# Performance work log

Hardware: AMD Instinct MI355X
Metric: run time of the kernel (lower is better)

Reference implementation:

```python
import jax, jax.numpy as jnp
import numpy as np
import math

B, S, D, H, F, E, K, L, V = 1, 2048, 768, 12, 1536, 8, 2, 2, 32000


def _ln(x, w, b, eps=1e-5):
    m = x.mean(-1, keepdims=True)
    v = ((x - m) ** 2).mean(-1, keepdims=True)
    return (x - m) / jnp.sqrt(v + eps) * w + b


def setup_inputs() -> dict:
    key = jax.random.key(0)
    ks = jax.random.split(key, 16)
    std = 0.02
    inp = {
        'tokens': jax.random.randint(ks[0], (B, S), 0, V),
        'emb': jax.random.normal(ks[1], (V, D), jnp.float32) * std,
        'qkv_w': jax.random.normal(ks[2], (L, 3 * D, D), jnp.float32) * std,
        'qkv_b': jax.random.normal(ks[3], (L, 3 * D), jnp.float32) * std,
        'out_w': jax.random.normal(ks[4], (L, D, D), jnp.float32) * std,
        'out_b': jax.random.normal(ks[5], (L, D), jnp.float32) * std,
        'ln1_w': jnp.ones((L, D), jnp.float32),
        'ln1_b': jax.random.normal(ks[6], (L, D), jnp.float32) * std,
        'ln2_w': jnp.ones((L, D), jnp.float32),
        'ln2_b': jax.random.normal(ks[7], (L, D), jnp.float32) * std,
        'gate_w': jax.random.normal(ks[8], (L, E, D), jnp.float32) * std,
        'eg_w': jax.random.normal(ks[9], (L, E, F, D), jnp.float32) * std,
        'eu_w': jax.random.normal(ks[10], (L, E, F, D), jnp.float32) * std,
        'ed_w': jax.random.normal(ks[11], (L, E, D, F), jnp.float32) * std,
        'rms_w': jnp.ones((D,), jnp.float32),
    }
    return inp


def reference(tokens, emb, qkv_w, qkv_b, out_w, out_b, ln1_w, ln1_b,
              ln2_w, ln2_b, gate_w, eg_w, eu_w, ed_w, rms_w):
    Dh = D // H
    x = emb[tokens] * math.sqrt(D)  # (B,S,D)
    for l in range(L):
        # --- MultiheadAttention (batch_first, no mask, eval) ---
        qkv = x @ qkv_w[l].T + qkv_b[l]
        q, k, v = jnp.split(qkv, 3, axis=-1)
        q = q.reshape(B, S, H, Dh).transpose(0, 2, 1, 3)
        k = k.reshape(B, S, H, Dh).transpose(0, 2, 1, 3)
        v = v.reshape(B, S, H, Dh).transpose(0, 2, 1, 3)
        att = jax.nn.softmax(jnp.einsum('bhqd,bhkd->bhqk', q, k) / math.sqrt(Dh), axis=-1)
        o = jnp.einsum('bhqk,bhkd->bhqd', att, v).transpose(0, 2, 1, 3).reshape(B, S, D)
        o = o @ out_w[l].T + out_b[l]
        x = _ln(x + o, ln1_w[l], ln1_b[l])
        # --- SimpleDeepseekV3MoE: top-k gate, softmax over top-k scores ---
        gs = jnp.einsum('bsd,ed->bse', x, gate_w[l])
        topv, topi = jax.lax.top_k(gs, K)
        tw = jax.nn.softmax(topv, axis=-1)  # (B,S,K)
        # dense per-expert combine weight (0 for unselected experts)
        ew = jnp.sum(jax.nn.one_hot(topi, E, dtype=x.dtype) * tw[..., None], axis=-2)  # (B,S,E)
        hg = jax.nn.silu(jnp.einsum('bsd,efd->bsef', x, eg_w[l]))
        hu = jnp.einsum('bsd,efd->bsef', x, eu_w[l])
        ye = jnp.einsum('bsef,edf->bsed', hg * hu, ed_w[l])
        moe = jnp.einsum('bsed,bse->bsd', ye, ew)
        x = _ln(x + moe, ln2_w[l], ln2_b[l])
    # final RMSNorm (torch default eps=None -> finfo eps)
    rms = jnp.sqrt(jnp.mean(x * x, axis=-1, keepdims=True) + jnp.finfo(x.dtype).eps)
    x = x / rms * rms_w
    logits = x @ emb.T  # tied lm_head
    return logits
```

## Files before the change

### kernel.cpp

```cpp
#include <hip/hip_runtime.h>

#define SQ   2048
#define DM   768
#define NHD  12
#define DHD  64
#define FF   1536
#define NE   8
#define NL   2
#define NV   32000

typedef __attribute__((ext_vector_type(8))) short bf16x8;
typedef __attribute__((ext_vector_type(4))) float f32x4;

__device__ __forceinline__ unsigned short f2bf(float f) {
  unsigned u = __float_as_uint(f);
  return (unsigned short)((u + 0x7fffu + ((u >> 16) & 1u)) >> 16);
}
__device__ __forceinline__ float bf2f(unsigned short h) {
  return __uint_as_float(((unsigned)h) << 16);
}

#define GLD16(ldsp, gp) __builtin_amdgcn_global_load_lds( \
    (const __attribute__((address_space(1))) void*)(gp),  \
    (__attribute__((address_space(3))) void*)(ldsp), 16, 0, 0)

__device__ __forceinline__ void conv8(const float* s, unsigned short* d) {
  float4 a = *(const float4*)s;
  float4 b = *(const float4*)(s + 4);
  int4 pk = make_int4(
      (int)((unsigned)f2bf(a.x) | ((unsigned)f2bf(a.y) << 16)),
      (int)((unsigned)f2bf(a.z) | ((unsigned)f2bf(a.w) << 16)),
      (int)((unsigned)f2bf(b.x) | ((unsigned)f2bf(b.y) << 16)),
      (int)((unsigned)f2bf(b.z) | ((unsigned)f2bf(b.w) << 16)));
  *(int4*)d = pk;
}

__global__ __launch_bounds__(256) void conv_embed_k(const int* __restrict__ tok,
    const float* __restrict__ emb, unsigned short* __restrict__ emb_bf,
    float* __restrict__ x, unsigned short* __restrict__ xbf,
    int* __restrict__ cnt) {
  int b = blockIdx.x;
  if (b < 12000) {
    size_t i = (size_t)(b * 256 + threadIdx.x) * 8;
    conv8(emb + i, emb_bf + i);
  } else {
    if (b == 12000 && threadIdx.x < NE) cnt[threadIdx.x] = 0;
    int idx = (b - 12000) * 256 + threadIdx.x;
    int s = idx / DM, d = idx % DM;
    float v = emb[(size_t)tok[s] * DM + d] * 27.712812921102035f;
    x[idx] = v;
    xbf[idx] = f2bf(v);
  }
}

__global__ __launch_bounds__(256) void conv5_k(const float* __restrict__ s0,
    const float* __restrict__ s1, const float* __restrict__ s2,
    const float* __restrict__ s3, const float* __restrict__ s4,
    unsigned short* __restrict__ d) {
  int b = blockIdx.x;
  const float* s; int sb;
  if (b < 864)        { s = s0; sb = b; }
  else if (b < 1152)  { s = s1; sb = b - 864; }
  else if (b < 5760)  { s = s2; sb = b - 1152; }
  else if (b < 10368) { s = s3; sb = b - 5760; }
  else                { s = s4; sb = b - 10368; }
  size_t di = (size_t)b * 2048 + threadIdx.x * 8;
  size_t si = (size_t)sb * 2048 + threadIdx.x * 8;
  conv8(s + si, d + di);
}

__global__ __launch_bounds__(512, 1) void gemmr_k(
    const unsigned short* __restrict__ A, long long lda,
    const unsigned short* __restrict__ B, long long ldb,
    float* __restrict__ C, long long ldc,
    int Kd, int mT)
{
  int nwg = gridDim.x, bid = blockIdx.x;
  int q = nwg >> 3, r = nwg & 7;
  int xcd = bid & 7, j = bid >> 3;
  int wid = (xcd < r ? xcd * (q + 1) : r * (q + 1) + (xcd - r) * q) + j;
  int mt = wid % mT, nt = wid / mT;
  int m0 = mt * 256, n0 = nt * 256;

  __shared__ __align__(16) unsigned short lds[4][2][8192];

  int t = threadIdx.x, w = t >> 6, lane = t & 63;
  int wm = w >> 2, wn = w & 3;
  int fr = lane & 15, ksg = lane >> 4;

  int srow = t >> 2;
  int schunk = ((t & 3) ^ ((srow >> 1) & 3)) * 8;
  const unsigned short* sa0 = A + (size_t)(m0 +       srow) * lda + schunk;
  const unsigned short* sa1 = A + (size_t)(m0 + 128 + srow) * lda + schunk;
  const unsigned short* sb0 = B + (size_t)(n0 +       srow) * ldb + schunk;
  const unsigned short* sb1 = B + (size_t)(n0 + 128 + srow) * ldb + schunk;
  int wofs = w * 512;

  int NS = Kd >> 5;
  f32x4 acc[8][4] = {};

#define STAGEV(s) { \
    int sl_ = (s) & 3; \
    long long ko_ = (long long)((s) >> 1) * 64 + ((s) & 1) * 32; \
    GLD16(&lds[sl_][0][wofs], sa0 + ko_); \
    GLD16(&lds[sl_][0][4096 + wofs], sa1 + ko_); \
    GLD16(&lds[sl_][1][wofs], sb0 + ko_); \
    GLD16(&lds[sl_][1][4096 + wofs], sb1 + ko_); }

  STAGEV(0);
  STAGEV(1);
  asm volatile("s_waitcnt vmcnt(4)" ::: "memory");
  __builtin_amdgcn_s_barrier();
  __builtin_amdgcn_sched_barrier(0);

  int ko = (ksg ^ ((fr >> 1) & 3)) * 8;
  for (int s = 0; s < NS; ++s) {
    int slot = s & 3;
    const unsigned short* Al = &lds[slot][0][0];
    const unsigned short* Bl = &lds[slot][1][0];
    bf16x8 af[8], bf[4];
    #pragma unroll
    for (int m = 0; m < 8; ++m)
      af[m] = *(const bf16x8*)&Al[(wm * 128 + m * 16 + fr) * 32 + ko];
    #pragma unroll
    for (int n = 0; n < 4; ++n)
      bf[n] = *(const bf16x8*)&Bl[(wn * 64 + n * 16 + fr) * 32 + ko];
    if (s + 2 < NS) STAGEV(s + 2);
    asm volatile("s_waitcnt lgkmcnt(0)" ::: "memory");
    __builtin_amdgcn_sched_barrier(0);
    __builtin_amdgcn_s_setprio(1);
    #pragma unroll
    for (int m = 0; m < 8; ++m)
      #pragma unroll
      for (int n = 0; n < 4; ++n)
        acc[m][n] = __builtin_amdgcn_mfma_f32_16x16x32_bf16(
            af[m], bf[n], acc[m][n], 0, 0, 0);
    __builtin_amdgcn_s_setprio(0);
    if (s + 1 < NS) {
      if (s + 2 < NS) asm volatile("s_waitcnt vmcnt(4)" ::: "memory");
      else            asm volatile("s_waitcnt vmcnt(0)" ::: "memory");
      __builtin_amdgcn_s_barrier();
      __builtin_amdgcn_sched_barrier(0);
    }
  }
#undef STAGEV

  int rb = ksg * 4;
  #pragma unroll
  for (int M = 0; M < 8; ++M)
    #pragma unroll
    for (int n = 0; n < 4; ++n)
      #pragma unroll
      for (int rr = 0; rr < 4; ++rr)
        C[(size_t)(m0 + wm * 128 + M * 16 + rb + rr) * ldc +
          (n0 + wn * 64 + n * 16 + fr)] = acc[M][n][rr];
}

template<bool GATHER, bool OBF16>
__global__ __launch_bounds__(512) void gemm256_k(
    const unsigned short* __restrict__ A, long long lda,
    const unsigned short* __restrict__ B, long long ldb, long long b_z,
    void* __restrict__ C, long long ldc, long long c_z,
    int M, int Kd, int mT, int nT, int Z, int zmod,
    const int* __restrict__ glist, long long gl_z,
    const int* __restrict__ cnt)
{
  int nwg = gridDim.x, bid = blockIdx.x;
  int q = nwg >> 3, r = nwg & 7;
  int xcd = bid & 7, j = bid >> 3;
  int wid = (xcd < r ? xcd * (q + 1) : r * (q + 1) + (xcd - r) * q) + j;
  int z = wid % Z; int rem = wid / Z;
  int mt = rem % mT, nt = rem / mT;
  int zz = z % zmod;
  int Mz = cnt ? cnt[zz] : M;
  int m0 = mt * 128, n0 = nt * 256;
  if (m0 >= Mz) return;
  (void)nT;

  const unsigned short* Bz = B + (size_t)z * b_z;

  __shared__ __align__(16) unsigned short lds[3 * 6 * 4096];

  int t = threadIdx.x, w = t >> 6, lane = t & 63;
  int wm = (w >> 2) * 64, wn = (w & 3) * 64;
  int fr = lane & 15, ksg = lane >> 4;
  int lrow = lane >> 3;
  int lchunk = ((lane & 7) ^ lrow) * 8;

  const unsigned short* sp[6];
  #pragma unroll
  for (int hh = 0; hh < 2; ++hh) {
    int gr = m0 + hh * 64 + w * 8 + lrow; if (gr >= Mz) gr = Mz - 1;
    int arow;
    if constexpr (GATHER) arow = glist[(size_t)zz * gl_z + gr]; else arow = gr;
    sp[hh] = A + (size_t)arow * lda + lchunk;
  }
  #pragma unroll
  for (int hh = 0; hh < 4; ++hh)
    sp[2 + hh] = Bz + (size_t)(n0 + hh * 64 + w * 8 + lrow) * ldb + lchunk;

  int rdA = (w >> 2) * 4096;
  int rdB = (2 + (w & 3)) * 4096;
  int stDst = w * 512;

  int rx = fr & 7;
  int off0 = (ksg ^ rx) * 8;
  int off1 = ((4 + ksg) ^ rx) * 8;

  int KT = Kd >> 6;
  f32x4 acc[4][4] = {};

  #pragma unroll
  for (int h = 0; h < 6; ++h)
    GLD16(&lds[h * 4096 + stDst], sp[h]);
  #pragma unroll
  for (int h = 0; h < 6; ++h)
    GLD16(&lds[(6 + h) * 4096 + stDst], sp[h] + 64);
  asm volatile("s_waitcnt vmcnt(6)" ::: "memory");
  __builtin_amdgcn_s_barrier();
  __builtin_amdgcn_sched_barrier(0);

  int buf = 0;
  for (int kt = 0; kt < KT; ++kt) {
    const unsigned short* Abl = &lds[buf * 6 * 4096 + rdA];
    const unsigned short* Bbl = &lds[buf * 6 * 4096 + rdB];
    int pf = (kt + 2 < KT);
    int pbuf = buf + 2; if (pbuf >= 3) pbuf -= 3;
    unsigned short* pd = &lds[pbuf * 6 * 4096 + stDst];
    long long koff = (long long)(kt + 2) * 64;

    if (pf) {
      GLD16(pd + 0 * 4096, sp[0] + koff);
      GLD16(pd + 1 * 4096, sp[1] + koff);
      GLD16(pd + 2 * 4096, sp[2] + koff);
    }
    {
      bf16x8 af[4], bv[4];
      #pragma unroll
      for (int m = 0; m < 4; ++m)
        af[m] = *(const bf16x8*)&Abl[(m * 16 + fr) * 64 + off0];
      #pragma unroll
      for (int n = 0; n < 4; ++n)
        bv[n] = *(const bf16x8*)&Bbl[(n * 16 + fr) * 64 + off0];
      __builtin_amdgcn_s_setprio(1);
      #pragma unroll
      for (int m = 0; m < 4; ++m)
        #pragma unroll
        for (int n = 0; n < 4; ++n)
          acc[m][n] = __builtin_amdgcn_mfma_f32_16x16x32_bf16(
              af[m], bv[n], acc[m][n], 0, 0, 0);
      __builtin_amdgcn_s_setprio(0);
    }
    if (pf) {
      GLD16(pd + 3 * 4096, sp[3] + koff);
      GLD16(pd + 4 * 4096, sp[4] + koff);
      GLD16(pd + 5 * 4096, sp[5] + koff);
    }
    {
      bf16x8 af[4], bv[4];
      #pragma unroll
      for (int m = 0; m < 4; ++m)
        af[m] = *(const bf16x8*)&Abl[(m * 16 + fr) * 64 + off1];
      #pragma unroll
      for (int n = 0; n < 4; ++n)
        bv[n] = *(const bf16x8*)&Bbl[(n * 16 + fr) * 64 + off1];
      __builtin_amdgcn_s_setprio(1);
      #pragma unroll
      for (int m = 0; m < 4; ++m)
        #pragma unroll
        for (int n = 0; n < 4; ++n)
          acc[m][n] = __builtin_amdgcn_mfma_f32_16x16x32_bf16(
              af[m], bv[n], acc[m][n], 0, 0, 0);
      __builtin_amdgcn_s_setprio(0);
    }
    if (pf) {
      asm volatile("s_waitcnt vmcnt(6)" ::: "memory");
    } else if (kt + 1 < KT) {
      asm volatile("s_waitcnt vmcnt(0)" ::: "memory");
    }
    __builtin_amdgcn_s_barrier();
    __builtin_amdgcn_sched_barrier(0);
    buf = buf + 1; if (buf == 3) buf = 0;
  }

  int rb = ksg * 4;
  #pragma unroll
  for (int m = 0; m < 4; ++m) {
    #pragma unroll
    for (int n = 0; n < 4; ++n) {
      #pragma unroll
      for (int rr = 0; rr < 4; ++rr) {
        int row = m0 + wm + m * 16 + rb + rr;
        if (row >= Mz) continue;
        size_t off = (size_t)z * c_z + (size_t)row * ldc +
                     (n0 + wn + n * 16 + fr);
        if constexpr (OBF16) ((unsigned short*)C)[off] = f2bf(acc[m][n][rr]);
        else                 ((float*)C)[off] = acc[m][n][rr];
      }
    }
  }
}

template<bool GATHER, bool BIAS, bool OBF16, bool VT>
__global__ __launch_bounds__(256) void gemm_k(
    const unsigned short* __restrict__ A, long long lda, long long a_z,
    const unsigned short* __restrict__ B, long long ldb, long long b_z,
    const float* __restrict__ bias,
    void* __restrict__ C, long long ldc, long long c_z,
    int M, int N, int Kd, float scale,
    const int* __restrict__ glist, long long gl_z,
    const int* __restrict__ cnt, int mT, int nT, int Z,
    unsigned short* __restrict__ vtout)
{
  int nwg = gridDim.x, bid = blockIdx.x;
  int q = nwg >> 3, r = nwg & 7;
  int xcd = bid & 7, j = bid >> 3;
  int wid = (xcd < r ? xcd * (q + 1) : r * (q + 1) + (xcd - r) * q) + j;
  int z = wid % Z; int rem = wid / Z;
  int mt = rem % mT, nt = rem / mT;

  int Mz = cnt ? cnt[z] : M;
  int m0 = mt * 128, n0 = nt * 128;
  if (m0 >= Mz) return;

  const unsigned short* Ab = A + (size_t)z * a_z;
  const unsigned short* Bb = B + (size_t)z * b_z;

  __shared__ __align__(16) unsigned short As[128 * 64];
  __shared__ __align__(16) unsigned short Bs[128 * 64];

  int t = threadIdx.x, w = t >> 6, lane = t & 63;
  int wm = (w >> 1) * 64, wn = (w & 1) * 64;
  int fr = lane & 15, ksg = lane >> 4;
  int lrow = lane >> 3;
  int lchunk = ((lane & 7) ^ lrow) * 8;

  const unsigned short* ap[4];
  const unsigned short* bp[4];
  unsigned short* la[4];
  unsigned short* lb[4];
  #pragma unroll
  for (int i = 0; i < 4; ++i) {
    int rrow = w * 32 + i * 8 + lrow;
    int gr = m0 + rrow; if (gr >= Mz) gr = Mz - 1;
    int arow; if constexpr (GATHER) arow = glist[(size_t)z * gl_z + gr]; else arow = gr;
    ap[i] = Ab + (size_t)arow * lda + lchunk;
    int br = n0 + rrow; if (br >= N) br = N - 1;
    bp[i] = Bb + (size_t)br * ldb + lchunk;
    la[i] = &As[(w * 32 + i * 8) * 64];
    lb[i] = &Bs[(w * 32 + i * 8) * 64];
  }

  int rx = fr & 7;
  int off0 = ((0 + ksg) ^ rx) * 8;
  int off1 = ((4 + ksg) ^ rx) * 8;

  f32x4 acc[4][4] = {};

  for (int k0 = 0; k0 < Kd; k0 += 64) {
    #pragma unroll
    for (int i = 0; i < 4; ++i) GLD16(la[i], ap[i] + k0);
    #pragma unroll
    for (int i = 0; i < 4; ++i) GLD16(lb[i], bp[i] + k0);
    __syncthreads();
    #pragma unroll
    for (int kb = 0; kb < 2; ++kb) {
      int offk = kb ? off1 : off0;
      bf16x8 af[4], bv[4];
      #pragma unroll
      for (int m = 0; m < 4; ++m)
        af[m] = *(const bf16x8*)&As[(wm + m * 16 + fr) * 64 + offk];
      #pragma unroll
      for (int n = 0; n < 4; ++n)
        bv[n] = *(const bf16x8*)&Bs[(wn + n * 16 + fr) * 64 + offk];
      #pragma unroll
      for (int m = 0; m < 4; ++m)
        #pragma unroll
        for (int n = 0; n < 4; ++n)
          acc[m][n] = __builtin_amdgcn_mfma_f32_16x16x32_bf16(
              af[m], bv[n], acc[m][n], 0, 0, 0);
    }
    __syncthreads();
  }

  int rb = ksg * 4;
  #pragma unroll
  for (int m = 0; m < 4; ++m) {
    #pragma unroll
    for (int n = 0; n < 4; ++n) {
      int col = n0 + wn + n * 16 + fr;
      if (col >= N) continue;
      #pragma unroll
      for (int rr = 0; rr < 4; ++rr) {
        int row = m0 + wm + m * 16 + rb + rr;
        if (row >= Mz) continue;
        float v = acc[m][n][rr] * scale;
        if constexpr (BIAS) v += bias[col];
        size_t off = (size_t)z * c_z + (size_t)row * ldc + col;
        if constexpr (OBF16) ((unsigned short*)C)[off] = f2bf(v);
        else                 ((float*)C)[off] = v;
        if constexpr (VT) {
          if (n0 >= 2 * DM)
            vtout[(size_t)(col - 2 * DM) * SQ + row] = f2bf(v);
        }
      }
    }
  }
}

__global__ __launch_bounds__(128) void flash_k(
    const unsigned short* __restrict__ qkv,
    const unsigned short* __restrict__ vt,
    unsigned short* __restrict__ o)
{
  int nwg = gridDim.x, bid = blockIdx.x;
  int cpx = nwg >> 3;
  int wid = (bid & 7) * cpx + (bid >> 3);
  int h  = wid >> 6;
  int qt = wid & 63;
  int q0 = qt * 32;

  __shared__ __align__(16) unsigned short Ks[128 * 64];
  __shared__ __align__(16) unsigned short Vs[128 * 64];
  __shared__ __align__(16) unsigned short Ps[2][16 * 136];

  int t = threadIdx.x, w = t >> 6, lane = t & 63;
  int fr = lane & 15, ksg = lane >> 4;
  int lrow = lane >> 3;
  int lchunk = ((lane & 7) ^ lrow) * 8;

  const unsigned short* qbase = qkv + (size_t)q0 * (3 * DM) + h * DHD;
  #pragma unroll
  for (int i = 0; i < 2; ++i) {
    int rrow = w * 16 + i * 8 + lrow;
    GLD16(&Ks[(w * 16 + i * 8) * 64], qbase + (size_t)rrow * (3 * DM) + lchunk);
  }
  __syncthreads();
  bf16x8 qf[2];
  {
    int row = w * 16 + fr, ph = fr & 7;
    qf[0] = *(const bf16x8*)&Ks[row * 64 + ((ksg ^ ph) * 8)];
    qf[1] = *(const bf16x8*)&Ks[row * 64 + (((4 + ksg) ^ ph) * 8)];
  }
  __syncthreads();

  const unsigned short* kbase = qkv + DM + h * DHD;
  const unsigned short* vb = vt + (size_t)(h * DHD) * SQ;

  f32x4 oacc[4] = {};
  float m_r[4] = {-1e30f, -1e30f, -1e30f, -1e30f};
  float l_r[4] = {0.f, 0.f, 0.f, 0.f};

  for (int kt = 0; kt < SQ / 128; ++kt) {
    int kk0 = kt * 128;
    #pragma unroll
    for (int i = 0; i < 8; ++i) {
      int rrow = w * 64 + i * 8 + lrow;
      GLD16(&Ks[(w * 64 + i * 8) * 64],
            kbase + (size_t)(kk0 + rrow) * (3 * DM) + lchunk);
    }
    #pragma unroll
    for (int i = 0; i < 8; ++i) {
      int p = w * 64 + i * 8 + lrow;
      GLD16(&Vs[(w * 64 + i * 8) * 64],
            vb + (size_t)(p >> 1) * SQ + kk0 + (p & 1) * 64 + lchunk);
    }
    __syncthreads();

    f32x4 sacc[8] = {};
    __builtin_amdgcn_s_setprio(1);
    #pragma unroll
    for (int kb = 0; kb < 2; ++kb) {
      #pragma unroll
      for (int n = 0; n < 8; ++n) {
        int row = n * 16 + fr;
        bf16x8 bvv = *(const bf16x8*)&Ks[row * 64 +
            (((kb * 4 + ksg) ^ (fr & 7)) * 8)];
        sacc[n] = __builtin_amdgcn_mfma_f32_16x16x32_bf16(
            qf[kb], bvv, sacc[n], 0, 0, 0);
      }
    }
    __builtin_amdgcn_s_setprio(0);

    #pragma unroll
    for (int r = 0; r < 4; ++r) {
      float mx = sacc[0][r];
      #pragma unroll
      for (int n = 1; n < 8; ++n) mx = fmaxf(mx, sacc[n][r]);
      mx = fmaxf(mx, __shfl_xor(mx, 1));
      mx = fmaxf(mx, __shfl_xor(mx, 2));
      mx = fmaxf(mx, __shfl_xor(mx, 4));
      mx = fmaxf(mx, __shfl_xor(mx, 8));
      float mn = fmaxf(m_r[r], mx * 0.125f);
      float resc = __expf(m_r[r] - mn);
      m_r[r] = mn;
      #pragma unroll
      for (int n = 0; n < 4; ++n) oacc[n][r] *= resc;
      float rs = 0.f;
      #pragma unroll
      for (int n = 0; n < 8; ++n) {
        float p = __expf(sacc[n][r] * 0.125f - mn);
        rs += p;
        Ps[w][(ksg * 4 + r) * 136 + n * 16 + fr] = f2bf(p);
      }
      rs += __shfl_xor(rs, 1);
      rs += __shfl_xor(rs, 2);
      rs += __shfl_xor(rs, 4);
      rs += __shfl_xor(rs, 8);
      l_r[r] = l_r[r] * resc + rs;
    }

    __builtin_amdgcn_s_setprio(1);
    #pragma unroll
    for (int ksi = 0; ksi < 4; ++ksi) {
      bf16x8 pa = *(const bf16x8*)&Ps[w][fr * 136 + ksi * 32 + ksg * 8];
      #pragma unroll
      for (int n = 0; n < 4; ++n) {
        int p = (n * 16 + fr) * 2 + (ksi >> 1);
        int c = (ksi & 1) * 4 + ksg;
        bf16x8 bvv = *(const bf16x8*)&Vs[p * 64 + ((c ^ (p & 7)) * 8)];
        oacc[n] = __builtin_amdgcn_mfma_f32_16x16x32_bf16(
            pa, bvv, oacc[n], 0, 0, 0);
      }
    }
    __builtin_amdgcn_s_setprio(0);
    __syncthreads();
  }

  unsigned short* ob = o + (size_t)(q0 + w * 16) * DM + h * DHD;
  #pragma unroll
  for (int r = 0; r < 4; ++r) {
    float invl = 1.f / l_r[r];
    int qrow = ksg * 4 + r;
    #pragma unroll
    for (int n = 0; n < 4; ++n)
      ob[(size_t)qrow * DM + n * 16 + fr] = f2bf(oacc[n][r] * invl);
  }
}

__global__ __launch_bounds__(256) void add_ln_gate_k(const float* __restrict__ xin,
    const float* __restrict__ add, const float* __restrict__ w,
    const float* __restrict__ b, const float* __restrict__ gw,
    float* __restrict__ xout, unsigned short* __restrict__ xbf,
    float* __restrict__ tw, int* __restrict__ ti, int* __restrict__ cnt,
    int* __restrict__ lists, int* __restrict__ slot) {
  int row = blockIdx.x, t = threadIdx.x;
  const float* xi = xin + (size_t)row * DM;
  const float* ai = add + (size_t)row * DM;
  float v[3]; float s = 0.f, sq = 0.f;
  #pragma unroll
  for (int i = 0; i < 3; ++i) {
    int idx = t + i * 256;
    v[i] = xi[idx] + ai[idx];
    s += v[i]; sq += v[i] * v[i];
  }
  #pragma unroll
  for (int o = 32; o; o >>= 1) { s += __shfl_xor(s, o); sq += __shfl_xor(sq, o); }
  __shared__ float rsm[4], rqm[4];
  __shared__ float gsm[4][NE];
  int wv = t >> 6, lane = t & 63;
  if (lane == 0) { rsm[wv] = s; rqm[wv] = sq; }
  __syncthreads();
  s = rsm[0] + rsm[1] + rsm[2] + rsm[3];
  sq = rqm[0] + rqm[1] + rqm[2] + rqm[3];
  float mean = s * (1.f / 768.f);
  float var = sq * (1.f / 768.f) - mean * mean;
  float inv = rsqrtf(var + 1e-5f);
  float* xo = xout + (size_t)row * DM;
  unsigned short* xb = xbf + (size_t)row * DM;
  float y[3];
  #pragma unroll
  for (int i = 0; i < 3; ++i) {
    int idx = t + i * 256;
    y[i] = (v[i] - mean) * inv * w[idx] + b[idx];
    xo[idx] = y[i]; xb[idx] = f2bf(y[i]);
  }
  float p[NE];
  #pragma unroll
  for (int e = 0; e < NE; ++e) {
    p[e] = y[0] * gw[e * DM + t] + y[1] * gw[e * DM + t + 256]
         + y[2] * gw[e * DM + t + 512];
    #pragma unroll
    for (int o = 32; o; o >>= 1) p[e] += __shfl_xor(p[e], o);
  }
  if (lane == 0) {
    #pragma unroll
    for (int e = 0; e < NE; ++e) gsm[wv][e] = p[e];
  }
  __syncthreads();
  if (t == 0) {
    float v0 = -1e30f, v1 = -1e30f; int i0 = 0, i1 = 0;
    #pragma unroll
    for (int e = 0; e < NE; ++e) {
      float g = gsm[0][e] + gsm[1][e] + gsm[2][e] + gsm[3][e];
      if (g > v0) { v1 = v0; i1 = i0; v0 = g; i0 = e; }
      else if (g > v1) { v1 = g; i1 = e; }
    }
    float e1 = expf(v1 - v0);
    float invs = 1.f / (1.f + e1);
    tw[row * 2] = invs; tw[row * 2 + 1] = e1 * invs;
    ti[row * 2] = i0;   ti[row * 2 + 1] = i1;
    int p0 = atomicAdd(&cnt[i0], 1); lists[i0 * SQ + p0] = row; slot[row * 2] = p0;
    int p1 = atomicAdd(&cnt[i1], 1); lists[i1 * SQ + p1] = row; slot[row * 2 + 1] = p1;
  }
}

__global__ __launch_bounds__(256) void silu_mul_k(unsigned short* __restrict__ hg,
    const unsigned short* __restrict__ hu, const int* __restrict__ cnt) {
  int e = blockIdx.y, sl = blockIdx.x;
  if (sl >= cnt[e]) return;
  size_t base = ((size_t)e * SQ + sl) * FF;
  int t = threadIdx.x;
  #pragma unroll
  for (int i = 0; i < FF / 256; ++i) {
    size_t idx = base + t + i * 256;
    float g = bf2f(hg[idx]);
    float u = bf2f(hu[idx]);
    float sv = g / (1.f + expf(-g));
    hg[idx] = f2bf(sv * u);
  }
}

template<bool FINAL>
__global__ __launch_bounds__(256) void combine_ln_k(const float* __restrict__ xin,
    const float* __restrict__ ye, const float* __restrict__ tw,
    const int* __restrict__ ti, const int* __restrict__ slot,
    const float* __restrict__ w, const float* __restrict__ b,
    const float* __restrict__ rw,
    float* __restrict__ xout, unsigned short* __restrict__ xbf,
    int* __restrict__ cnt) {
  int row = blockIdx.x, t = threadIdx.x;
  if (!FINAL && row < NE && t == 0) cnt[row] = 0;
  int e0 = ti[row * 2], e1 = ti[row * 2 + 1];
  int p0 = slot[row * 2], p1 = slot[row * 2 + 1];
  float w0 = tw[row * 2], w1 = tw[row * 2 + 1];
  const float* y0 = ye + ((size_t)e0 * SQ + p0) * DM;
  const float* y1 = ye + ((size_t)e1 * SQ + p1) * DM;
  const float* xi = xin + (size_t)row * DM;
  float v[3]; float s = 0.f, sq = 0.f;
  #pragma unroll
  for (int i = 0; i < 3; ++i) {
    int idx = t + i * 256;
    v[i] = xi[idx] + w0 * y0[idx] + w1 * y1[idx];
    s += v[i]; sq += v[i] * v[i];
  }
  #pragma unroll
  for (int o = 32; o; o >>= 1) { s += __shfl_xor(s, o); sq += __shfl_xor(sq, o); }
  __shared__ float rsm[4], rqm[4];
  int wv = t >> 6;
  if ((t & 63) == 0) { rsm[wv] = s; rqm[wv] = sq; }
  __syncthreads();
  s = rsm[0] + rsm[1] + rsm[2] + rsm[3];
  sq = rqm[0] + rqm[1] + rqm[2] + rqm[3];
  float mean = s * (1.f / 768.f);
  float var = sq * (1.f / 768.f) - mean * mean;
  float inv = rsqrtf(var + 1e-5f);
  unsigned short* xb = xbf + (size_t)row * DM;
  float y[3];
  #pragma unroll
  for (int i = 0; i < 3; ++i) {
    int idx = t + i * 256;
    y[i] = (v[i] - mean) * inv * w[idx] + b[idx];
  }
  if constexpr (!FINAL) {
    float* xo = xout + (size_t)row * DM;
    #pragma unroll
    for (int i = 0; i < 3; ++i) {
      int idx = t + i * 256;
      xo[idx] = y[i]; xb[idx] = f2bf(y[i]);
    }
  } else {
    float sq2 = y[0] * y[0] + y[1] * y[1] + y[2] * y[2];
    #pragma unroll
    for (int o = 32; o; o >>= 1) sq2 += __shfl_xor(sq2, o);
    __syncthreads();
    if ((t & 63) == 0) rqm[wv] = sq2;
    __syncthreads();
    sq2 = rqm[0] + rqm[1] + rqm[2] + rqm[3];
    float inv2 = rsqrtf(sq2 * (1.f / 768.f) + 1.1920929e-07f);
    #pragma unroll
    for (int i = 0; i < 3; ++i) {
      int idx = t + i * 256;
      xb[idx] = f2bf(y[i] * inv2 * rw[idx]);
    }
  }
}

extern "C" void kernel_launch(void* const* d_in, const int* in_sizes, int n_in,
                              void* d_out, int out_size, void* d_ws, size_t ws_size,
                              hipStream_t stream) {
  (void)in_sizes; (void)n_in; (void)out_size; (void)ws_size;
  const int*   tokens = (const int*)d_in[0];
  const float* emb    = (const float*)d_in[1];
  const float* qkv_w  = (const float*)d_in[2];
  const float* qkv_b  = (const float*)d_in[3];
  const float* out_w  = (const float*)d_in[4];
  const float* out_b  = (const float*)d_in[5];
  const float* ln1_w  = (const float*)d_in[6];
  const float* ln1_b  = (const float*)d_in[7];
  const float* ln2_w  = (const float*)d_in[8];
  const float* ln2_b  = (const float*)d_in[9];
  const float* gate_w = (const float*)d_in[10];
  const float* eg_w   = (const float*)d_in[11];
  const float* eu_w   = (const float*)d_in[12];
  const float* ed_w   = (const float*)d_in[13];
  const float* rms_w  = (const float*)d_in[14];
  float* out = (float*)d_out;

  char* wsb = (char*)d_ws;
  float*          x_f    = (float*)(wsb + 0);
  unsigned short* x_bf   = (unsigned short*)(wsb + 6291456);
  unsigned short* qkv_bf = (unsigned short*)(wsb + 9437184);
  unsigned short* vt     = (unsigned short*)(wsb + 18874368);
  unsigned short* o_bf   = (unsigned short*)(wsb + 22020096);
  float*          tmp_f  = (float*)(wsb + 25165824);
  float*          tw     = (float*)(wsb + 31457280);
  int*            ti     = (int*)(wsb + 31473664);
  int*            cnt    = (int*)(wsb + 31490048);
  int*            lists  = (int*)(wsb + 31490304);
  int*            slot   = (int*)(wsb + 31555840);
  unsigned short* emb_bf = (unsigned short*)(wsb + 31572224);
  unsigned short* wbf    = (unsigned short*)(wsb + 80724224);
  unsigned short* hg     = (unsigned short*)(wsb + 142065920);
  unsigned short* hu     = (unsigned short*)(wsb + 142065920 + 50331648);
  float*          ye     = (float*)(wsb + 142065920 + 50331648);

  unsigned short* qw_bf = wbf;
  unsigned short* ow_bf = wbf + 1769472;
  unsigned short* eg_bf = wbf + 2359296;
  unsigned short* ed_bf = wbf + 21233664;

  conv_embed_k<<<18144, 256, 0, stream>>>(tokens, emb, emb_bf, x_f, x_bf, cnt);

  for (int l = 0; l < NL; ++l) {
    const float* qw = qkv_w + (size_t)l * 3 * DM * DM;
    const float* qb = qkv_b + (size_t)l * 3 * DM;
    const float* ow = out_w + (size_t)l * DM * DM;
    const float* ob = out_b + (size_t)l * DM;
    const float* gw = gate_w + (size_t)l * NE * DM;
    const float* egw = eg_w + (size_t)l * NE * FF * DM;
    const float* euw = eu_w + (size_t)l * NE * FF * DM;
    const float* edw = ed_w + (size_t)l * NE * DM * FF;

    conv5_k<<<14976, 256, 0, stream>>>(qw, ow, egw, euw, edw, qw_bf);

    gemm_k<false, true, true, true><<<16 * 18, 256, 0, stream>>>(
        x_bf, DM, 0, qw_bf, DM, 0, qb, qkv_bf, 3 * DM, 0,
        SQ, 3 * DM, DM, 1.f, nullptr, 0, nullptr, 16, 18, 1, vt);

    flash_k<<<NHD * 64, 128, 0, stream>>>(qkv_bf, vt, o_bf);

    gemm_k<false, true, false, false><<<16 * 6, 256, 0, stream>>>(
        o_bf, DM, 0, ow_bf, DM, 0, ob, tmp_f, DM, 0,
        SQ, DM, DM, 1.f, nullptr, 0, nullptr, 16, 6, 1, nullptr);

    add_ln_gate_k<<<SQ, 256, 0, stream>>>(x_f, tmp_f, ln1_w + l * DM,
        ln1_b + l * DM, gw, x_f, x_bf, tw, ti, cnt, lists, slot);

    gemm256_k<true, true><<<16 * 6 * 16, 512, 0, stream>>>(
        x_bf, DM, eg_bf, DM, (long long)FF * DM,
        hg, FF, (long long)SQ * FF,
        SQ, DM, 16, 6, 16, 8, lists, SQ, cnt);

    silu_mul_k<<<dim3(SQ, NE), 256, 0, stream>>>(hg, hu, cnt);

    gemm_k<false, false, false, false><<<16 * 6 * NE, 256, 0, stream>>>(
        hg, FF, (long long)SQ * FF, ed_bf, FF, (long long)DM * FF, nullptr,
        ye, DM, (long long)SQ * DM,
        SQ, DM, FF, 1.f, nullptr, 0, cnt, 16, 6, NE, nullptr);

    if (l == NL - 1)
      combine_ln_k<true><<<SQ, 256, 0, stream>>>(x_f, ye, tw, ti, slot,
          ln2_w + l * DM, ln2_b + l * DM, rms_w, x_f, x_bf, cnt);
    else
      combine_ln_k<false><<<SQ, 256, 0, stream>>>(x_f, ye, tw, ti, slot,
          ln2_w + l * DM, ln2_b + l * DM, rms_w, x_f, x_bf, cnt);
  }

  gemmr_k<<<8 * 125, 512, 0, stream>>>(
      x_bf, DM, emb_bf, DM, out, NV, DM, 8);
}
```

Measured before the change: 761.6 us.

## Fuse gate and up expert GEMMs with SiLU-multiply epilogue into one kernel

```diff
diff --git a/kernel.cpp b/kernel.cpp
--- a/kernel.cpp
+++ b/kernel.cpp
@@ -154,151 +154,6 @@
       for (int rr = 0; rr < 4; ++rr)
         C[(size_t)(m0 + wm * 128 + M * 16 + rb + rr) * ldc +
           (n0 + wn * 64 + n * 16 + fr)] = acc[M][n][rr];
-}
-
-template<bool GATHER, bool OBF16>
-__global__ __launch_bounds__(512) void gemm256_k(
-    const unsigned short* __restrict__ A, long long lda,
-    const unsigned short* __restrict__ B, long long ldb, long long b_z,
-    void* __restrict__ C, long long ldc, long long c_z,
-    int M, int Kd, int mT, int nT, int Z, int zmod,
-    const int* __restrict__ glist, long long gl_z,
-    const int* __restrict__ cnt)
-{
-  int nwg = gridDim.x, bid = blockIdx.x;
-  int q = nwg >> 3, r = nwg & 7;
-  int xcd = bid & 7, j = bid >> 3;
-  int wid = (xcd < r ? xcd * (q + 1) : r * (q + 1) + (xcd - r) * q) + j;
-  int z = wid % Z; int rem = wid / Z;
-  int mt = rem % mT, nt = rem / mT;
-  int zz = z % zmod;
-  int Mz = cnt ? cnt[zz] : M;
-  int m0 = mt * 128, n0 = nt * 256;
-  if (m0 >= Mz) return;
-  (void)nT;
-
-  const unsigned short* Bz = B + (size_t)z * b_z;
-
-  __shared__ __align__(16) unsigned short lds[3 * 6 * 4096];
-
-  int t = threadIdx.x, w = t >> 6, lane = t & 63;
-  int wm = (w >> 2) * 64, wn = (w & 3) * 64;
-  int fr = lane & 15, ksg = lane >> 4;
-  int lrow = lane >> 3;
-  int lchunk = ((lane & 7) ^ lrow) * 8;
-
-  const unsigned short* sp[6];
-  #pragma unroll
-  for (int hh = 0; hh < 2; ++hh) {
-    int gr = m0 + hh * 64 + w * 8 + lrow; if (gr >= Mz) gr = Mz - 1;
-    int arow;
-    if constexpr (GATHER) arow = glist[(size_t)zz * gl_z + gr]; else arow = gr;
-    sp[hh] = A + (size_t)arow * lda + lchunk;
-  }
-  #pragma unroll
-  for (int hh = 0; hh < 4; ++hh)
-    sp[2 + hh] = Bz + (size_t)(n0 + hh * 64 + w * 8 + lrow) * ldb + lchunk;
-
-  int rdA = (w >> 2) * 4096;
-  int rdB = (2 + (w & 3)) * 4096;
-  int stDst = w * 512;
-
-  int rx = fr & 7;
-  int off0 = (ksg ^ rx) * 8;
-  int off1 = ((4 + ksg) ^ rx) * 8;
-
-  int KT = Kd >> 6;
-  f32x4 acc[4][4] = {};
-
-  #pragma unroll
-  for (int h = 0; h < 6; ++h)
-    GLD16(&lds[h * 4096 + stDst], sp[h]);
-  #pragma unroll
-  for (int h = 0; h < 6; ++h)
-    GLD16(&lds[(6 + h) * 4096 + stDst], sp[h] + 64);
-  asm volatile("s_waitcnt vmcnt(6)" ::: "memory");
-  __builtin_amdgcn_s_barrier();
-  __builtin_amdgcn_sched_barrier(0);
-
-  int buf = 0;
-  for (int kt = 0; kt < KT; ++kt) {
-    const unsigned short* Abl = &lds[buf * 6 * 4096 + rdA];
-    const unsigned short* Bbl = &lds[buf * 6 * 4096 + rdB];
-    int pf = (kt + 2 < KT);
-    int pbuf = buf + 2; if (pbuf >= 3) pbuf -= 3;
-    unsigned short* pd = &lds[pbuf * 6 * 4096 + stDst];
-    long long koff = (long long)(kt + 2) * 64;
-
-    if (pf) {
-      GLD16(pd + 0 * 4096, sp[0] + koff);
-      GLD16(pd + 1 * 4096, sp[1] + koff);
-      GLD16(pd + 2 * 4096, sp[2] + koff);
-    }
-    {
-      bf16x8 af[4], bv[4];
-      #pragma unroll
-      for (int m = 0; m < 4; ++m)
-        af[m] = *(const bf16x8*)&Abl[(m * 16 + fr) * 64 + off0];
-      #pragma unroll
-      for (int n = 0; n < 4; ++n)
-        bv[n] = *(const bf16x8*)&Bbl[(n * 16 + fr) * 64 + off0];
-      __builtin_amdgcn_s_setprio(1);
-      #pragma unroll
-      for (int m = 0; m < 4; ++m)
-        #pragma unroll
-        for (int n = 0; n < 4; ++n)
-          acc[m][n] = __builtin_amdgcn_mfma_f32_16x16x32_bf16(
-              af[m], bv[n], acc[m][n], 0, 0, 0);
-      __builtin_amdgcn_s_setprio(0);
-    }
-    if (pf) {
-      GLD16(pd + 3 * 4096, sp[3] + koff);
-      GLD16(pd + 4 * 4096, sp[4] + koff);
-      GLD16(pd + 5 * 4096, sp[5] + koff);
-    }
-    {
-      bf16x8 af[4], bv[4];
-      #pragma unroll
-      for (int m = 0; m < 4; ++m)
-        af[m] = *(const bf16x8*)&Abl[(m * 16 + fr) * 64 + off1];
-      #pragma unroll
-      for (int n = 0; n < 4; ++n)
-        bv[n] = *(const bf16x8*)&Bbl[(n * 16 + fr) * 64 + off1];
-      __builtin_amdgcn_s_setprio(1);
-      #pragma unroll
-      for (int m = 0; m < 4; ++m)
-        #pragma unroll
-        for (int n = 0; n < 4; ++n)
-          acc[m][n] = __builtin_amdgcn_mfma_f32_16x16x32_bf16(
-              af[m], bv[n], acc[m][n], 0, 0, 0);
-      __builtin_amdgcn_s_setprio(0);
-    }
-    if (pf) {
-      asm volatile("s_waitcnt vmcnt(6)" ::: "memory");
-    } else if (kt + 1 < KT) {
-      asm volatile("s_waitcnt vmcnt(0)" ::: "memory");
-    }
-    __builtin_amdgcn_s_barrier();
-    __builtin_amdgcn_sched_barrier(0);
-    buf = buf + 1; if (buf == 3) buf = 0;
-  }
-
-  int rb = ksg * 4;
-  #pragma unroll
-  for (int m = 0; m < 4; ++m) {
-    #pragma unroll
-    for (int n = 0; n < 4; ++n) {
-      #pragma unroll
-      for (int rr = 0; rr < 4; ++rr) {
-        int row = m0 + wm + m * 16 + rb + rr;
-        if (row >= Mz) continue;
-        size_t off = (size_t)z * c_z + (size_t)row * ldc +
-                     (n0 + wn + n * 16 + fr);
-        if constexpr (OBF16) ((unsigned short*)C)[off] = f2bf(acc[m][n][rr]);
-        else                 ((float*)C)[off] = acc[m][n][rr];
-      }
-    }
-  }
 }
 
 template<bool GATHER, bool BIAS, bool OBF16, bool VT>
@@ -408,6 +263,118 @@
   }
 }
 
+__global__ __launch_bounds__(256) void gemm_dual_k(
+    const unsigned short* __restrict__ A, long long lda,
+    const unsigned short* __restrict__ Bg, const unsigned short* __restrict__ Bu,
+    long long ldb, long long b_z,
+    unsigned short* __restrict__ C, long long ldc, long long c_z,
+    int M, int N, int Kd,
+    const int* __restrict__ glist, long long gl_z,
+    const int* __restrict__ cnt, int mT, int nT, int Z)
+{
+  int nwg = gridDim.x, bid = blockIdx.x;
+  int q = nwg >> 3, r = nwg & 7;
+  int xcd = bid & 7, j = bid >> 3;
+  int wid = (xcd < r ? xcd * (q + 1) : r * (q + 1) + (xcd - r) * q) + j;
+  int z = wid % Z; int rem = wid / Z;
+  int mt = rem % mT, nt = rem / mT;
+
+  int Mz = cnt[z];
+  int m0 = mt * 128, n0 = nt * 128;
+  if (m0 >= Mz) return;
+
+  const unsigned short* Bgz = Bg + (size_t)z * b_z;
+  const unsigned short* Buz = Bu + (size_t)z * b_z;
+
+  __shared__ __align__(16) unsigned short As[128 * 64];
+  __shared__ __align__(16) unsigned short Bgs[128 * 64];
+  __shared__ __align__(16) unsigned short Bus[128 * 64];
+
+  int t = threadIdx.x, w = t >> 6, lane = t & 63;
+  int wm = (w >> 1) * 64, wn = (w & 1) * 64;
+  int fr = lane & 15, ksg = lane >> 4;
+  int lrow = lane >> 3;
+  int lchunk = ((lane & 7) ^ lrow) * 8;
+
+  const unsigned short* ap[4];
+  const unsigned short* bgp[4];
+  const unsigned short* bup[4];
+  #pragma unroll
+  for (int i = 0; i < 4; ++i) {
+    int rrow = w * 32 + i * 8 + lrow;
+    int gr = m0 + rrow; if (gr >= Mz) gr = Mz - 1;
+    int arow = glist[(size_t)z * gl_z + gr];
+    ap[i] = A + (size_t)arow * lda + lchunk;
+    int br = n0 + rrow;
+    bgp[i] = Bgz + (size_t)br * ldb + lchunk;
+    bup[i] = Buz + (size_t)br * ldb + lchunk;
+  }
+
+  int rx = fr & 7;
+  int off0 = ((0 + ksg) ^ rx) * 8;
+  int off1 = ((4 + ksg) ^ rx) * 8;
+
+  f32x4 accg[4][4] = {};
+  f32x4 accu[4][4] = {};
+
+  for (int k0 = 0; k0 < Kd; k0 += 64) {
+    #pragma unroll
+    for (int i = 0; i < 4; ++i) GLD16(&As[(w * 32 + i * 8) * 64], ap[i] + k0);
+    #pragma unroll
+    for (int i = 0; i < 4; ++i) GLD16(&Bgs[(w * 32 + i * 8) * 64], bgp[i] + k0);
+    #pragma unroll
+    for (int i = 0; i < 4; ++i) GLD16(&Bus[(w * 32 + i * 8) * 64], bup[i] + k0);
+    __syncthreads();
+    #pragma unroll
+    for (int kb = 0; kb < 2; ++kb) {
+      int offk = kb ? off1 : off0;
+      bf16x8 af[4], bg[4], bu[4];
+      #pragma unroll
+      for (int m = 0; m < 4; ++m)
+        af[m] = *(const bf16x8*)&As[(wm + m * 16 + fr) * 64 + offk];
+      #pragma unroll
+      for (int n = 0; n < 4; ++n)
+        bg[n] = *(const bf16x8*)&Bgs[(wn + n * 16 + fr) * 64 + offk];
+      #pragma unroll
+      for (int n = 0; n < 4; ++n)
+        bu[n] = *(const bf16x8*)&Bus[(wn + n * 16 + fr) * 64 + offk];
+      __builtin_amdgcn_s_setprio(1);
+      #pragma unroll
+      for (int m = 0; m < 4; ++m)
+        #pragma unroll
+        for (int n = 0; n < 4; ++n)
+          accg[m][n] = __builtin_amdgcn_mfma_f32_16x16x32_bf16(
+              af[m], bg[n], accg[m][n], 0, 0, 0);
+      #pragma unroll
+      for (int m = 0; m < 4; ++m)
+        #pragma unroll
+        for (int n = 0; n < 4; ++n)
+          accu[m][n] = __builtin_amdgcn_mfma_f32_16x16x32_bf16(
+              af[m], bu[n], accu[m][n], 0, 0, 0);
+      __builtin_amdgcn_s_setprio(0);
+    }
+    __syncthreads();
+  }
+
+  int rb = ksg * 4;
+  #pragma unroll
+  for (int m = 0; m < 4; ++m) {
+    #pragma unroll
+    for (int n = 0; n < 4; ++n) {
+      int col = n0 + wn + n * 16 + fr;
+      #pragma unroll
+      for (int rr = 0; rr < 4; ++rr) {
+        int row = m0 + wm + m * 16 + rb + rr;
+        if (row >= Mz) continue;
+        float g = accg[m][n][rr];
+        float u = accu[m][n][rr];
+        float sv = g / (1.f + __expf(-g));
+        C[(size_t)z * c_z + (size_t)row * ldc + col] = f2bf(sv * u);
+      }
+    }
+  }
+}
+
 __global__ __launch_bounds__(128) void flash_k(
     const unsigned short* __restrict__ qkv,
     const unsigned short* __restrict__ vt,
@@ -602,22 +569,6 @@
     ti[row * 2] = i0;   ti[row * 2 + 1] = i1;
     int p0 = atomicAdd(&cnt[i0], 1); lists[i0 * SQ + p0] = row; slot[row * 2] = p0;
     int p1 = atomicAdd(&cnt[i1], 1); lists[i1 * SQ + p1] = row; slot[row * 2 + 1] = p1;
-  }
-}
-
-__global__ __launch_bounds__(256) void silu_mul_k(unsigned short* __restrict__ hg,
-    const unsigned short* __restrict__ hu, const int* __restrict__ cnt) {
-  int e = blockIdx.y, sl = blockIdx.x;
-  if (sl >= cnt[e]) return;
-  size_t base = ((size_t)e * SQ + sl) * FF;
-  int t = threadIdx.x;
-  #pragma unroll
-  for (int i = 0; i < FF / 256; ++i) {
-    size_t idx = base + t + i * 256;
-    float g = bf2f(hg[idx]);
-    float u = bf2f(hu[idx]);
-    float sv = g / (1.f + expf(-g));
-    hg[idx] = f2bf(sv * u);
   }
 }
 
@@ -721,13 +672,13 @@
   int*            slot   = (int*)(wsb + 31555840);
   unsigned short* emb_bf = (unsigned short*)(wsb + 31572224);
   unsigned short* wbf    = (unsigned short*)(wsb + 80724224);
-  unsigned short* hg     = (unsigned short*)(wsb + 142065920);
-  unsigned short* hu     = (unsigned short*)(wsb + 142065920 + 50331648);
+  unsigned short* hh     = (unsigned short*)(wsb + 142065920);
   float*          ye     = (float*)(wsb + 142065920 + 50331648);
 
   unsigned short* qw_bf = wbf;
   unsigned short* ow_bf = wbf + 1769472;
   unsigned short* eg_bf = wbf + 2359296;
+  unsigned short* eu_bf = wbf + 11796480;
   unsigned short* ed_bf = wbf + 21233664;
 
   conv_embed_k<<<18144, 256, 0, stream>>>(tokens, emb, emb_bf, x_f, x_bf, cnt);
@@ -757,15 +708,13 @@
     add_ln_gate_k<<<SQ, 256, 0, stream>>>(x_f, tmp_f, ln1_w + l * DM,
         ln1_b + l * DM, gw, x_f, x_bf, tw, ti, cnt, lists, slot);
 
-    gemm256_k<true, true><<<16 * 6 * 16, 512, 0, stream>>>(
-        x_bf, DM, eg_bf, DM, (long long)FF * DM,
-        hg, FF, (long long)SQ * FF,
-        SQ, DM, 16, 6, 16, 8, lists, SQ, cnt);
-
-    silu_mul_k<<<dim3(SQ, NE), 256, 0, stream>>>(hg, hu, cnt);
+    gemm_dual_k<<<16 * 12 * NE, 256, 0, stream>>>(
+        x_bf, DM, eg_bf, eu_bf, DM, (long long)FF * DM,
+        hh, FF, (long long)SQ * FF,
+        SQ, FF, DM, lists, SQ, cnt, 16, 12, NE);
 
     gemm_k<false, false, false, false><<<16 * 6 * NE, 256, 0, stream>>>(
-        hg, FF, (long long)SQ * FF, ed_bf, FF, (long long)DM * FF, nullptr,
+        hh, FF, (long long)SQ * FF, ed_bf, FF, (long long)DM * FF, nullptr,
         ye, DM, (long long)SQ * DM,
         SQ, DM, FF, 1.f, nullptr, 0, cnt, 16, 6, NE, nullptr);
 
```

New measurement: 848.1 us. 1.11x slower.
